# Kernel optimization log

Measured on AMD Instinct MI355X. Metric: run time of the kernel, lower is better.

Reference implementation:

```python
import jax, jax.numpy as jnp
import numpy as np

B, O, L, T = 1024, 50, 20, 10
D, H, V = 64, 128, 49688
DM, FF = 2 * H, 4 * H  # transformer d_model=256, ffn=512


def _ln(x, g, b, eps=1e-5):
    m = x.mean(-1, keepdims=True)
    v = ((x - m) ** 2).mean(-1, keepdims=True)
    return (x - m) / jnp.sqrt(v + eps) * g + b


def _mha(x, in_w, in_b, out_w, out_b, nh):
    # x: [..., S, d]; torch nn.MultiheadAttention with packed qkv in_proj
    lead, S, d = x.shape[:-2], x.shape[-2], x.shape[-1]
    hd = d // nh
    qkv = x @ in_w.T + in_b
    q, k, v = jnp.split(qkv, 3, axis=-1)
    q = q.reshape(*lead, S, nh, hd)
    k = k.reshape(*lead, S, nh, hd)
    v = v.reshape(*lead, S, nh, hd)
    sc = jnp.einsum('...qhd,...khd->...hqk', q, k) / jnp.sqrt(jnp.asarray(hd, x.dtype))
    a = jax.nn.softmax(sc, axis=-1)
    o = jnp.einsum('...hqk,...khd->...qhd', a, v).reshape(*lead, S, d)
    return o @ out_w.T + out_b


def _gru_dir(x_seq, wi, wh, bi, bh):
    # x_seq: [O, B, D] -> outputs [O, B, H]; PyTorch GRU cell equations
    def step(h, x):
        gi = x @ wi.T + bi
        gh = h @ wh.T + bh
        i_r, i_z, i_n = jnp.split(gi, 3, axis=-1)
        h_r, h_z, h_n = jnp.split(gh, 3, axis=-1)
        r = jax.nn.sigmoid(i_r + h_r)
        z = jax.nn.sigmoid(i_z + h_z)
        n = jnp.tanh(i_n + r * h_n)
        h2 = (1.0 - z) * n + z * h
        return h2, h2
    h0 = jnp.zeros((x_seq.shape[1], wh.shape[1]), x_seq.dtype)
    _, ys = jax.lax.scan(step, h0, x_seq)
    return ys


def setup_inputs() -> dict:
    key = jax.random.key(0)
    ks = jax.random.split(key, 20)
    rn = lambda k, shape: jax.random.normal(k, shape, jnp.float32) * 0.05
    return {
        'order_history': jax.random.randint(ks[0], (B, O, L), 0, V, jnp.int32),
        'days_between': jax.random.uniform(ks[1], (B, T), jnp.float32) * 30.0,
        'days_since_last': jax.random.uniform(ks[2], (B,), jnp.float32) * 30.0,
        'item_emb': rn(ks[3], (V + 1, D)).at[0].set(0.0),  # padding_idx=0
        'ia_in_w': rn(ks[4], (3 * D, D)), 'ia_in_b': jnp.zeros(3 * D),
        'ia_out_w': rn(ks[5], (D, D)), 'ia_out_b': jnp.zeros(D),
        'gf_wi': rn(ks[6], (3 * H, D)), 'gf_wh': rn(ks[7], (3 * H, H)),
        'gf_bi': jnp.zeros(3 * H), 'gf_bh': jnp.zeros(3 * H),
        'gb_wi': rn(ks[8], (3 * H, D)), 'gb_wh': rn(ks[9], (3 * H, H)),
        'gb_bi': jnp.zeros(3 * H), 'gb_bh': jnp.zeros(3 * H),
        'ta_in_w': rn(ks[10], (3 * DM, DM)), 'ta_in_b': jnp.zeros(3 * DM),
        'ta_out_w': rn(ks[11], (DM, DM)), 'ta_out_b': jnp.zeros(DM),
        't_ln1_g': jnp.ones(DM), 't_ln1_b': jnp.zeros(DM),
        't_ln2_g': jnp.ones(DM), 't_ln2_b': jnp.zeros(DM),
        't_ff1_w': rn(ks[12], (FF, DM)), 't_ff1_b': jnp.zeros(FF),
        't_ff2_w': rn(ks[13], (DM, FF)), 't_ff2_b': jnp.zeros(DM),
        'te1_w': rn(ks[14], (H // 4, 2)), 'te1_b': jnp.zeros(H // 4),
        'te_ln1_g': jnp.ones(H // 4), 'te_ln1_b': jnp.zeros(H // 4),
        'te2_w': rn(ks[15], (H // 2, H // 4)), 'te2_b': jnp.zeros(H // 2),
        'te_ln2_g': jnp.ones(H // 2), 'te_ln2_b': jnp.zeros(H // 2),
        'c_w': rn(ks[16], (H, DM + H // 2)), 'c_b': jnp.zeros(H),
        'c_ln_g': jnp.ones(H), 'c_ln_b': jnp.zeros(H),
    }


def reference(order_history, days_between, days_since_last, item_emb,
              ia_in_w, ia_in_b, ia_out_w, ia_out_b,
              gf_wi, gf_wh, gf_bi, gf_bh, gb_wi, gb_wh, gb_bi, gb_bh,
              ta_in_w, ta_in_b, ta_out_w, ta_out_b,
              t_ln1_g, t_ln1_b, t_ln2_g, t_ln2_b,
              t_ff1_w, t_ff1_b, t_ff2_w, t_ff2_b,
              te1_w, te1_b, te_ln1_g, te_ln1_b, te2_w, te2_b, te_ln2_g, te_ln2_b,
              c_w, c_b, c_ln_g, c_ln_b):
    # per-order item embedding + self-attention + mean pool (batched over B,O)
    E = item_emb[order_history]                            # [B,O,L,D]
    A = _mha(E, ia_in_w, ia_in_b, ia_out_w, ia_out_b, 4)   # [B,O,L,D]
    order_emb = A.mean(axis=2)                             # [B,O,D]
    # bidirectional GRU over order sequence
    x = jnp.transpose(order_emb, (1, 0, 2))                # [O,B,D]
    yf = _gru_dir(x, gf_wi, gf_wh, gf_bi, gf_bh)
    yb = _gru_dir(x[::-1], gb_wi, gb_wh, gb_bi, gb_bh)[::-1]
    g = jnp.transpose(jnp.concatenate([yf, yb], axis=-1), (1, 0, 2))  # [B,O,2H]
    # post-norm TransformerEncoderLayer (dropout inactive at eval)
    sa = _mha(g, ta_in_w, ta_in_b, ta_out_w, ta_out_b, 4)
    h1 = _ln(g + sa, t_ln1_g, t_ln1_b)
    ff = jax.nn.relu(h1 @ t_ff1_w.T + t_ff1_b) @ t_ff2_w.T + t_ff2_b
    h2 = _ln(h1 + ff, t_ln2_g, t_ln2_b)
    order_enc = h2.mean(axis=1)                            # [B,2H]
    # temporal features: mean(days_between), recency (days_std is unused in original)
    feat = jnp.stack([days_between.mean(axis=1), days_since_last], axis=1)  # [B,2]
    t1 = jax.nn.relu(_ln(feat @ te1_w.T + te1_b, te_ln1_g, te_ln1_b))
    t2 = jax.nn.relu(_ln(t1 @ te2_w.T + te2_b, te_ln2_g, te_ln2_b))        # [B,H//2]
    u = jnp.concatenate([order_enc, t2], axis=1)           # [B,2H+H//2]
    return jax.nn.relu(_ln(u @ c_w.T + c_b, c_ln_g, c_ln_b))  # [B,H]
```

## Files before the change

### kernel.cpp

```cpp
#include <hip/hip_runtime.h>


#define B_ 1024
#define O_ 50
#define VROWS 49689
#define VPAD  49792

typedef __attribute__((ext_vector_type(8))) short  short8v;
typedef __attribute__((ext_vector_type(4))) short  short4v;
typedef __attribute__((ext_vector_type(8))) unsigned short ushort8v;
typedef __attribute__((ext_vector_type(4))) unsigned short ushort4v;
typedef __attribute__((ext_vector_type(4))) float f32x4;

__device__ __forceinline__ float sig_(float x)  { return 1.0f / (1.0f + __expf(-x)); }
__device__ __forceinline__ float tanh_(float x) { return 2.0f / (1.0f + __expf(-2.0f * x)) - 1.0f; }

__device__ __forceinline__ unsigned short f2bf(float f) {
  union { float f; unsigned int u; } v; v.f = f;
  unsigned int r = v.u + 0x7FFFu + ((v.u >> 16) & 1u);
  return (unsigned short)(r >> 16);
}
__device__ __forceinline__ float bf2f(unsigned short u) {
  union { unsigned int u; float f; } v; v.u = ((unsigned int)u) << 16;
  return v.f;
}
__device__ __forceinline__ unsigned int pk2bf(float lo, float hi) {
  return (unsigned int)f2bf(lo) | ((unsigned int)f2bf(hi) << 16);
}

__global__ void k_transpose(const float* __restrict__ src, float* __restrict__ dst, int R, int C) {
  int i = blockIdx.x * 256 + threadIdx.x;
  if (i < R * C) {
    int r = i / C, c = i - r * C;
    dst[c * R + r] = src[i];
  }
}

__global__ void k_f32bf16(const float* __restrict__ src, unsigned short* __restrict__ dst, int n) {
  int i = blockIdx.x * 256 + threadIdx.x;
  if (i < n) dst[i] = f2bf(src[i]);
}

__global__ void k_fill_u16(unsigned short* __restrict__ dst, int n) {
  int i = blockIdx.x * 256 + threadIdx.x;
  if (i < n) dst[i] = 0;
}

__global__ void k_pad_bias(const float* __restrict__ src, float* __restrict__ dst,
                           int ns, int nt) {
  int i = blockIdx.x * 256 + threadIdx.x;
  if (i < nt) dst[i] = (i < ns) ? src[i] : 0.f;
}

__global__ void k_cat_bias(const float* __restrict__ a, const float* __restrict__ b,
                           float* __restrict__ dst) {
  int i = blockIdx.x * 256 + threadIdx.x;
  if (i < 768) dst[i] = (i < 384) ? a[i] : b[i - 384];
}

template<int RELU>
__global__ __launch_bounds__(256) void k_gemm128(
    const unsigned short* __restrict__ A, int lda,
    const unsigned short* __restrict__ W, int K,
    const float* __restrict__ bias,
    unsigned short* __restrict__ C, int ldc, int Mclamp)
{
  __shared__ unsigned short As[128 * 40];
  __shared__ unsigned short Bs[128 * 40];
  int n0 = blockIdx.x * 128, m0 = blockIdx.y * 128;
  int t = threadIdx.x, wv = t >> 6, lane = t & 63;
  int fr = lane & 15, kg = lane >> 4;
  int wr = wv >> 1, wc = wv & 1;
  int sr = t >> 1, sc = (t & 1) * 16;

  f32x4 acc[4][4];
#pragma unroll
  for (int mi = 0; mi < 4; ++mi)
#pragma unroll
    for (int ni = 0; ni < 4; ++ni) acc[mi][ni] = (f32x4){0.f, 0.f, 0.f, 0.f};

  int arow = m0 + sr; if (arow >= Mclamp) arow = Mclamp - 1;
  const unsigned short* ga = &A[(size_t)arow * lda + sc];
  const unsigned short* gw = &W[(size_t)(n0 + sr) * K + sc];

  for (int k0 = 0; k0 < K; k0 += 32) {
    ushort8v a0 = *(const ushort8v*)(ga + k0);
    ushort8v a1 = *(const ushort8v*)(ga + k0 + 8);
    ushort8v b0 = *(const ushort8v*)(gw + k0);
    ushort8v b1 = *(const ushort8v*)(gw + k0 + 8);
    __syncthreads();
    *(ushort8v*)&As[sr * 40 + sc]     = a0;
    *(ushort8v*)&As[sr * 40 + sc + 8] = a1;
    *(ushort8v*)&Bs[sr * 40 + sc]     = b0;
    *(ushort8v*)&Bs[sr * 40 + sc + 8] = b1;
    __syncthreads();
    short8v af[4], bfv[4];
#pragma unroll
    for (int mi = 0; mi < 4; ++mi)
      af[mi] = *(const short8v*)&As[(wr * 64 + mi * 16 + fr) * 40 + kg * 8];
#pragma unroll
    for (int ni = 0; ni < 4; ++ni)
      bfv[ni] = *(const short8v*)&Bs[(wc * 64 + ni * 16 + fr) * 40 + kg * 8];
#pragma unroll
    for (int mi = 0; mi < 4; ++mi)
#pragma unroll
      for (int ni = 0; ni < 4; ++ni)
        acc[mi][ni] = __builtin_amdgcn_mfma_f32_16x16x32_bf16(af[mi], bfv[ni], acc[mi][ni], 0, 0, 0);
  }

#pragma unroll
  for (int ni = 0; ni < 4; ++ni) {
    int col = n0 + wc * 64 + ni * 16 + fr;
    float bb = bias[col];
#pragma unroll
    for (int mi = 0; mi < 4; ++mi) {
#pragma unroll
      for (int r = 0; r < 4; ++r) {
        int row = m0 + wr * 64 + mi * 16 + kg * 4 + r;
        float v = acc[mi][ni][r] + bb;
        if (RELU) v = fmaxf(v, 0.f);
        C[(size_t)row * ldc + col] = f2bf(v);
      }
    }
  }
}

__global__ __launch_bounds__(256) void k_item_fused(
    const int* __restrict__ oh,
    const unsigned short* __restrict__ QKVall ,
    const float* __restrict__ wo , const float* __restrict__ bob,
    unsigned short* __restrict__ X )
{
  __shared__ __align__(16) unsigned short QKs[2][20][144];
  __shared__ __align__(16) unsigned short VTs[2][64][36];
  __shared__ __align__(16) unsigned short Ps[4][24][36];
  __shared__ __align__(16) float mAs[2][68];
  __shared__ int ids[2][20];

  int t = threadIdx.x, wv = t >> 6, lane = t & 63;
  int fr = lane & 15, lg = lane >> 4;
  int pr = wv >> 1, half = wv & 1;

  if (t < 40) ids[t / 20][t % 20] = oh[(size_t)(blockIdx.x * 2 + t / 20) * 20 + (t % 20)];
  {
    unsigned int* vz = (unsigned int*)&VTs[t >> 7][(t >> 1) & 63][20 + (t & 1) * 8];
    vz[0] = 0; vz[1] = 0; vz[2] = 0; vz[3] = 0;
    for (int e = t; e < 288; e += 256) {
      int w2 = e / 72, rem = e - w2 * 72;
      *(unsigned int*)&Ps[w2][20 + rem / 18][(rem - (rem / 18) * 18) * 2] = 0;
    }
  }
  __syncthreads();

  for (int e = t; e < 640; e += 256) {
    int pp = e / 320, rem = e - pp * 320;
    int row = rem >> 4, ch = (rem & 15) * 8;
    const unsigned short* src = QKVall + (size_t)ids[pp][row] * 256 + ch;
    *(ushort8v*)&QKs[pp][row][ch] = *(const ushort8v*)src;
  }
  for (int e = t; e < 1280; e += 256) {
    int pp = e / 640, rem = e - pp * 640;
    int jp = rem >> 6, c = rem & 63;
    unsigned int u0 = QKVall[(size_t)ids[pp][2 * jp] * 256 + 128 + c];
    unsigned int u1 = QKVall[(size_t)ids[pp][2 * jp + 1] * 256 + 128 + c];
    *(unsigned int*)&VTs[pp][c][2 * jp] = u0 | (u1 << 16);
  }
  __syncthreads();

  int rj1 = (fr + 16 < 20) ? fr + 16 : 19;
  bool iv1 = fr < 4;
  int pr1 = iv1 ? 16 + fr : 20;
#pragma unroll
  for (int hi = 0; hi < 2; ++hi) {
    int h = half * 2 + hi;
    short8v aK0, aK1, bQ0, bQ1;
    {
      short8v z = {0,0,0,0,0,0,0,0};
      aK0 = z; aK1 = z; bQ0 = z; bQ1 = z;
    }
    if (lg < 2) {
      aK0 = *(const short8v*)&QKs[pr][fr][64 + h * 16 + lg * 8];
      aK1 = *(const short8v*)&QKs[pr][rj1][64 + h * 16 + lg * 8];
      bQ0 = *(const short8v*)&QKs[pr][fr][h * 16 + lg * 8];
      bQ1 = *(const short8v*)&QKs[pr][rj1][h * 16 + lg * 8];
    }
    f32x4 s00 = {0.f,0.f,0.f,0.f}, s01 = {0.f,0.f,0.f,0.f};
    f32x4 s10 = {0.f,0.f,0.f,0.f}, s11 = {0.f,0.f,0.f,0.f};
    s00 = __builtin_amdgcn_mfma_f32_16x16x32_bf16(aK0, bQ0, s00, 0, 0, 0);
    s01 = __builtin_amdgcn_mfma_f32_16x16x32_bf16(aK0, bQ1, s01, 0, 0, 0);
    s10 = __builtin_amdgcn_mfma_f32_16x16x32_bf16(aK1, bQ0, s10, 0, 0, 0);
    s11 = __builtin_amdgcn_mfma_f32_16x16x32_bf16(aK1, bQ1, s11, 0, 0, 0);

    float e00[4], e01[4], e10[4], e11[4];
    float d0 = 0.f, d1 = 0.f;
#pragma unroll
    for (int r = 0; r < 4; ++r) {
      int j1 = 16 + lg * 4 + r;
      bool jv1 = j1 < 20;
      float v00 = __expf(0.25f * s00[r]);
      float v01 = iv1 ? __expf(0.25f * s01[r]) : 0.f;
      float v10 = jv1 ? __expf(0.25f * s10[r]) : 0.f;
      float v11 = (jv1 && iv1) ? __expf(0.25f * s11[r]) : 0.f;
      e00[r] = v00; e01[r] = v01; e10[r] = v10; e11[r] = v11;
      d0 += v00 + v10; d1 += v01 + v11;
    }
    d0 += __shfl_xor(d0, 16, 64); d0 += __shfl_xor(d0, 32, 64);
    d1 += __shfl_xor(d1, 16, 64); d1 += __shfl_xor(d1, 32, 64);
    float inv0 = __fdividef(1.f, d0);
    float inv1 = iv1 ? __fdividef(1.f, d1) : 0.f;

    *(unsigned int*)&Ps[wv][fr][lg * 4]          = pk2bf(e00[0]*inv0, e00[1]*inv0);
    *(unsigned int*)&Ps[wv][fr][lg * 4 + 2]      = pk2bf(e00[2]*inv0, e00[3]*inv0);
    *(unsigned int*)&Ps[wv][fr][16 + lg * 4]     = pk2bf(e10[0]*inv0, e10[1]*inv0);
    *(unsigned int*)&Ps[wv][fr][16 + lg * 4 + 2] = pk2bf(e10[2]*inv0, e10[3]*inv0);
    if (iv1) {
      *(unsigned int*)&Ps[wv][16 + fr][lg * 4]          = pk2bf(e01[0]*inv1, e01[1]*inv1);
      *(unsigned int*)&Ps[wv][16 + fr][lg * 4 + 2]      = pk2bf(e01[2]*inv1, e01[3]*inv1);
      *(unsigned int*)&Ps[wv][16 + fr][16 + lg * 4]     = pk2bf(e11[0]*inv1, e11[1]*inv1);
      *(unsigned int*)&Ps[wv][16 + fr][16 + lg * 4 + 2] = pk2bf(e11[2]*inv1, e11[3]*inv1);
    }

    short8v pa0, pa1, bV;
    {
      short4v l0 = *(const short4v*)&Ps[wv][fr][lg * 8];
      short4v h0 = *(const short4v*)&Ps[wv][fr][lg * 8 + 4];
      short4v l1 = *(const short4v*)&Ps[wv][pr1][lg * 8];
      short4v h1 = *(const short4v*)&Ps[wv][pr1][lg * 8 + 4];
      short4v lv = *(const short4v*)&VTs[pr][h * 16 + fr][lg * 8];
      short4v hv = *(const short4v*)&VTs[pr][h * 16 + fr][lg * 8 + 4];
      pa0[0]=l0[0]; pa0[1]=l0[1]; pa0[2]=l0[2]; pa0[3]=l0[3];
      pa0[4]=h0[0]; pa0[5]=h0[1]; pa0[6]=h0[2]; pa0[7]=h0[3];
      pa1[0]=l1[0]; pa1[1]=l1[1]; pa1[2]=l1[2]; pa1[3]=l1[3];
      pa1[4]=h1[0]; pa1[5]=h1[1]; pa1[6]=h1[2]; pa1[7]=h1[3];
      bV[0]=lv[0]; bV[1]=lv[1]; bV[2]=lv[2]; bV[3]=lv[3];
      bV[4]=hv[0]; bV[5]=hv[1]; bV[6]=hv[2]; bV[7]=hv[3];
    }
    f32x4 m20 = {0.f,0.f,0.f,0.f}, m21 = {0.f,0.f,0.f,0.f};
    m20 = __builtin_amdgcn_mfma_f32_16x16x32_bf16(pa0, bV, m20, 0, 0, 0);
    m21 = __builtin_amdgcn_mfma_f32_16x16x32_bf16(pa1, bV, m21, 0, 0, 0);

    float sm = m20[0] + m20[1] + m20[2] + m20[3];
    if (lg == 0) sm += m21[0] + m21[1] + m21[2] + m21[3];
    sm += __shfl_xor(sm, 16, 64);
    sm += __shfl_xor(sm, 32, 64);
    if (lg == 0) mAs[pr][h * 16 + fr] = sm * 0.05f;
  }
  __syncthreads();

  if (t < 128) {
    int p2 = t >> 6, col = t & 63;
    float acc = bob[col];
    const float* wrow = &wo[(size_t)col * 64];
    for (int k = 0; k < 64; k += 4) {
      float4 m4 = *(const float4*)&mAs[p2][k];
      float4 w4 = *(const float4*)(wrow + k);
      acc += m4.x * w4.x + m4.y * w4.y + m4.z * w4.z + m4.w * w4.w;
    }
    X[(size_t)(blockIdx.x * 2 + p2) * 64 + col] = f2bf(acc);
  }
}

__global__ __launch_bounds__(512) void k_gru_mfma(
    const unsigned short* __restrict__ GI,
    const unsigned short* __restrict__ whf,
    const unsigned short* __restrict__ whb,
    const float* __restrict__ bh_f, const float* __restrict__ bh_b,
    unsigned short* __restrict__ G )
{
  __shared__ unsigned short hsb[16][136];
  __shared__ float ah[4][392];

  int bid = blockIdx.x;
  int dir = bid >> 8;
  int rg  = bid & 255;
  const unsigned short* wh = dir ? whb : whf;
  const float* bh = dir ? bh_b : bh_f;

  int t = threadIdx.x;
  int w = t >> 6, lane = t & 63;
  int fr = lane & 15, kg = lane >> 4;

  short8v bfr[3][4];
#pragma unroll
  for (int n = 0; n < 3; ++n)
#pragma unroll
    for (int kf = 0; kf < 4; ++kf)
      bfr[n][kf] = *(const short8v*)&wh[(size_t)(w * 48 + n * 16 + fr) * 128 + kf * 32 + kg * 8];

  for (int e = t; e < 16 * 136; e += 512) ((unsigned short*)hsb)[e] = 0;

  int grow = t >> 7, gc = t & 127;
  float bh0 = bh[gc], bh1 = bh[128 + gc], bh2 = bh[256 + gc];
  float hold = 0.f;
  const unsigned short* gip = &GI[(size_t)(rg * 4 + grow) * 50 * 768 + dir * 384];
  unsigned short* gout = &G[((size_t)(rg * 4 + grow) * 50) * 256 + dir * 128 + gc];

  __syncthreads();

  int o0 = dir ? 49 : 0;
  unsigned short c0v = gip[(size_t)o0 * 768 + gc];
  unsigned short c1v = gip[(size_t)o0 * 768 + 128 + gc];
  unsigned short c2v = gip[(size_t)o0 * 768 + 256 + gc];

  for (int s = 0; s < 50; ++s) {
    int o  = dir ? 49 - s : s;
    unsigned short n0v = 0, n1v = 0, n2v = 0;
    if (s < 49) {
      int on = dir ? 48 - s : s + 1;
      n0v = gip[(size_t)on * 768 + gc];
      n1v = gip[(size_t)on * 768 + 128 + gc];
      n2v = gip[(size_t)on * 768 + 256 + gc];
    }

    short8v a0 = *(const short8v*)&hsb[fr][0 * 32 + kg * 8];
    short8v a1 = *(const short8v*)&hsb[fr][1 * 32 + kg * 8];
    short8v a2 = *(const short8v*)&hsb[fr][2 * 32 + kg * 8];
    short8v a3 = *(const short8v*)&hsb[fr][3 * 32 + kg * 8];

    f32x4 acc0 = {0.f,0.f,0.f,0.f}, acc1 = {0.f,0.f,0.f,0.f}, acc2 = {0.f,0.f,0.f,0.f};
    acc0 = __builtin_amdgcn_mfma_f32_16x16x32_bf16(a0, bfr[0][0], acc0, 0, 0, 0);
    acc1 = __builtin_amdgcn_mfma_f32_16x16x32_bf16(a0, bfr[1][0], acc1, 0, 0, 0);
    acc2 = __builtin_amdgcn_mfma_f32_16x16x32_bf16(a0, bfr[2][0], acc2, 0, 0, 0);
    acc0 = __builtin_amdgcn_mfma_f32_16x16x32_bf16(a1, bfr[0][1], acc0, 0, 0, 0);
    acc1 = __builtin_amdgcn_mfma_f32_16x16x32_bf16(a1, bfr[1][1], acc1, 0, 0, 0);
    acc2 = __builtin_amdgcn_mfma_f32_16x16x32_bf16(a1, bfr[2][1], acc2, 0, 0, 0);
    acc0 = __builtin_amdgcn_mfma_f32_16x16x32_bf16(a2, bfr[0][2], acc0, 0, 0, 0);
    acc1 = __builtin_amdgcn_mfma_f32_16x16x32_bf16(a2, bfr[1][2], acc1, 0, 0, 0);
    acc2 = __builtin_amdgcn_mfma_f32_16x16x32_bf16(a2, bfr[2][2], acc2, 0, 0, 0);
    acc0 = __builtin_amdgcn_mfma_f32_16x16x32_bf16(a3, bfr[0][3], acc0, 0, 0, 0);
    acc1 = __builtin_amdgcn_mfma_f32_16x16x32_bf16(a3, bfr[1][3], acc1, 0, 0, 0);
    acc2 = __builtin_amdgcn_mfma_f32_16x16x32_bf16(a3, bfr[2][3], acc2, 0, 0, 0);

    if (kg == 0) {
#pragma unroll
      for (int r = 0; r < 4; ++r) {
        ah[r][w * 48 + 0 * 16 + fr] = acc0[r];
        ah[r][w * 48 + 1 * 16 + fr] = acc1[r];
        ah[r][w * 48 + 2 * 16 + fr] = acc2[r];
      }
    }
    __syncthreads();

    float ai0 = bf2f(c0v), ai1 = bf2f(c1v), ai2 = bf2f(c2v);
    float ah0 = ah[grow][gc] + bh0;
    float ah1 = ah[grow][128 + gc] + bh1;
    float ah2 = ah[grow][256 + gc] + bh2;
    float rr = sig_(ai0 + ah0);
    float zz = sig_(ai1 + ah1);
    float nn = tanh_(ai2 + rr * ah2);
    float h2 = (1.f - zz) * nn + zz * hold;
    hold = h2;
    unsigned short hb = f2bf(h2);
    hsb[grow][gc] = hb;
    gout[(size_t)o * 256] = hb;
    c0v = n0v; c1v = n1v; c2v = n2v;
    __syncthreads();
  }
}

__global__ __launch_bounds__(256) void k_attn_core(unsigned short* __restrict__ BIG)
{
  __shared__ __align__(16) float qs[50][68], ks[50][68], vs[50][68];
  __shared__ float P[50][52];
  int bl = blockIdx.x >> 2, h = blockIdx.x & 3;
  int t = threadIdx.x;
  size_t base = (size_t)bl * 50 * 768;
  int hc = h * 64;

  for (int e = t; e < 800; e += 256) {
    int row = e >> 4, c4 = (e & 15) * 4;
    ushort4v q4 = *(const ushort4v*)&BIG[base + (size_t)row * 768 + hc + c4];
    ushort4v k4 = *(const ushort4v*)&BIG[base + (size_t)row * 768 + 256 + hc + c4];
    ushort4v v4 = *(const ushort4v*)&BIG[base + (size_t)row * 768 + 512 + hc + c4];
#pragma unroll
    for (int j = 0; j < 4; ++j) {
      qs[row][c4 + j] = bf2f(q4[j]);
      ks[row][c4 + j] = bf2f(k4[j]);
      vs[row][c4 + j] = bf2f(v4[j]);
    }
  }
  __syncthreads();

  for (int e = t; e < 2500; e += 256) {
    int i = e / 50, j = e - (e / 50) * 50;
    float d = 0.f;
#pragma unroll
    for (int k = 0; k < 64; k += 4) {
      float4 q = *(const float4*)&qs[i][k];
      float4 kk = *(const float4*)&ks[j][k];
      d += q.x * kk.x + q.y * kk.y + q.z * kk.z + q.w * kk.w;
    }
    P[i][j] = d * 0.125f;
  }
  __syncthreads();

  {
    int l = t & 31, rslot = t >> 5;
    for (int i0 = 0; i0 < 50; i0 += 8) {
      int i = i0 + rslot;
      if (i < 50) {
        float p1 = P[i][l];
        float p2 = (l < 18) ? P[i][l + 32] : -1e30f;
        float m = fmaxf(p1, p2);
#pragma unroll
        for (int d2 = 1; d2 < 32; d2 <<= 1) m = fmaxf(m, __shfl_xor(m, d2, 32));
        float e1 = __expf(p1 - m);
        float e2 = (l < 18) ? __expf(p2 - m) : 0.f;
        float s = e1 + e2;
#pragma unroll
        for (int d2 = 1; d2 < 32; d2 <<= 1) s += __shfl_xor(s, d2, 32);
        float inv = __fdividef(1.f, s);
        P[i][l] = e1 * inv;
        if (l < 18) P[i][l + 32] = e2 * inv;
      }
    }
  }
  __syncthreads();
  for (int e = t; e < 1600; e += 256) {
    int i = e >> 5, c2 = (e & 31) * 2;
    float a0 = 0.f, a1 = 0.f;
    for (int j = 0; j < 50; ++j) {
      float pv = P[i][j];
      a0 += pv * vs[j][c2];
      a1 += pv * vs[j][c2 + 1];
    }
    *(unsigned int*)&BIG[base + (size_t)i * 768 + hc + c2] = pk2bf(a0, a1);
  }
}

__global__ __launch_bounds__(256) void k_ln_res(
    const unsigned short* __restrict__ res, const unsigned short* __restrict__ add,
    int addld, unsigned short* __restrict__ dst,
    const float* __restrict__ g, const float* __restrict__ bt)
{
  int row = blockIdx.x * 4 + (threadIdx.x >> 6);
  int lane = threadIdx.x & 63;
  int c = lane * 4;
  ushort4v rv = *(const ushort4v*)&res[(size_t)row * 256 + c];
  ushort4v av = *(const ushort4v*)&add[(size_t)row * addld + c];
  float x0 = bf2f(rv[0]) + bf2f(av[0]);
  float x1 = bf2f(rv[1]) + bf2f(av[1]);
  float x2 = bf2f(rv[2]) + bf2f(av[2]);
  float x3 = bf2f(rv[3]) + bf2f(av[3]);
  float s = x0 + x1 + x2 + x3;
  float sq = x0 * x0 + x1 * x1 + x2 * x2 + x3 * x3;
#pragma unroll
  for (int d = 1; d < 64; d <<= 1) { s += __shfl_xor(s, d, 64); sq += __shfl_xor(sq, d, 64); }
  float m = s * (1.f / 256.f);
  float var = sq * (1.f / 256.f) - m * m;
  float rs = rsqrtf(var + 1e-5f);
  float4 gv = *(const float4*)&g[c];
  float4 bv = *(const float4*)&bt[c];
  ushort4v ov;
  ov[0] = f2bf((x0 - m) * rs * gv.x + bv.x);
  ov[1] = f2bf((x1 - m) * rs * gv.y + bv.y);
  ov[2] = f2bf((x2 - m) * rs * gv.z + bv.z);
  ov[3] = f2bf((x3 - m) * rs * gv.w + bv.w);
  *(ushort4v*)&dst[(size_t)row * 256 + c] = ov;
}

__global__ __launch_bounds__(256) void k_heads(
    const unsigned short* __restrict__ H2 ,
    const float* __restrict__ daysb, const float* __restrict__ dayss,
    const float* __restrict__ te1_w, const float* __restrict__ te1_b,
    const float* __restrict__ ln1g, const float* __restrict__ ln1b,
    const float* __restrict__ te2_w, const float* __restrict__ te2_b,
    const float* __restrict__ ln2g, const float* __restrict__ ln2b,
    const float* __restrict__ cWT ,
    const float* __restrict__ c_b, const float* __restrict__ clng,
    const float* __restrict__ clnb, float* __restrict__ out)
{
  __shared__ float oe[256];
  __shared__ float feat[2];
  __shared__ float s1[32], s2[64], pre[128], stat[2];
  int b = blockIdx.x, t = threadIdx.x;
  {
    float s = 0.f;
    for (int o = 0; o < 50; ++o) s += bf2f(H2[((size_t)b * 50 + o) * 256 + t]);
    oe[t] = s * 0.02f;
  }
  if (t == 0) {
    float f0 = 0.f;
    for (int i = 0; i < 10; ++i) f0 += daysb[b * 10 + i];
    feat[0] = f0 * 0.1f;
    feat[1] = dayss[b];
  }
  __syncthreads();
  if (t < 32) s1[t] = te1_b[t] + feat[0] * te1_w[2 * t] + feat[1] * te1_w[2 * t + 1];
  __syncthreads();
  if (t == 0) {
    float s = 0.f; for (int j = 0; j < 32; ++j) s += s1[j];
    float m = s * (1.f / 32.f);
    float v = 0.f; for (int j = 0; j < 32; ++j) { float d = s1[j] - m; v += d * d; }
    stat[0] = m; stat[1] = rsqrtf(v * (1.f / 32.f) + 1e-5f);
  }
  __syncthreads();
  if (t < 32) s1[t] = fmaxf((s1[t] - stat[0]) * stat[1] * ln1g[t] + ln1b[t], 0.f);
  __syncthreads();
  if (t < 64) {
    float a = te2_b[t];
    for (int k = 0; k < 32; ++k) a += s1[k] * te2_w[t * 32 + k];
    s2[t] = a;
  }
  __syncthreads();
  if (t == 0) {
    float s = 0.f; for (int j = 0; j < 64; ++j) s += s2[j];
    float m = s * (1.f / 64.f);
    float v = 0.f; for (int j = 0; j < 64; ++j) { float d = s2[j] - m; v += d * d; }
    stat[0] = m; stat[1] = rsqrtf(v * (1.f / 64.f) + 1e-5f);
  }
  __syncthreads();
  if (t < 64) s2[t] = fmaxf((s2[t] - stat[0]) * stat[1] * ln2g[t] + ln2b[t], 0.f);
  __syncthreads();
  if (t < 128) {
    float p = c_b[t];
    for (int k = 0; k < 256; ++k) p += oe[k] * cWT[k * 128 + t];
    for (int k = 0; k < 64; ++k)  p += s2[k] * cWT[(256 + k) * 128 + t];
    pre[t] = p;
  }
  __syncthreads();
  if (t == 0) {
    float s = 0.f; for (int j = 0; j < 128; ++j) s += pre[j];
    float m = s * (1.f / 128.f);
    float v = 0.f; for (int j = 0; j < 128; ++j) { float d = pre[j] - m; v += d * d; }
    stat[0] = m; stat[1] = rsqrtf(v * (1.f / 128.f) + 1e-5f);
  }
  __syncthreads();
  if (t < 128)
    out[(size_t)b * 128 + t] = fmaxf((pre[t] - stat[0]) * stat[1] * clng[t] + clnb[t], 0.f);
}

extern "C" void kernel_launch(void* const* d_in, const int* in_sizes, int n_in,
                              void* d_out, int out_size, void* d_ws, size_t ws_size,
                              hipStream_t stream)
{
  const int*   oh       = (const int*)d_in[0];
  const float* daysb    = (const float*)d_in[1];
  const float* dayss    = (const float*)d_in[2];
  const float* emb      = (const float*)d_in[3];
  const float* ia_in_w  = (const float*)d_in[4];
  const float* ia_in_b  = (const float*)d_in[5];
  const float* ia_out_w = (const float*)d_in[6];
  const float* ia_out_b = (const float*)d_in[7];
  const float* gf_wi = (const float*)d_in[8];
  const float* gf_wh = (const float*)d_in[9];
  const float* gf_bi = (const float*)d_in[10];
  const float* gf_bh = (const float*)d_in[11];
  const float* gb_wi = (const float*)d_in[12];
  const float* gb_wh = (const float*)d_in[13];
  const float* gb_bi = (const float*)d_in[14];
  const float* gb_bh = (const float*)d_in[15];
  const float* ta_in_w  = (const float*)d_in[16];
  const float* ta_in_b  = (const float*)d_in[17];
  const float* ta_out_w = (const float*)d_in[18];
  const float* ta_out_b = (const float*)d_in[19];
  const float* t_ln1_g = (const float*)d_in[20];
  const float* t_ln1_b = (const float*)d_in[21];
  const float* t_ln2_g = (const float*)d_in[22];
  const float* t_ln2_b = (const float*)d_in[23];
  const float* t_ff1_w = (const float*)d_in[24];
  const float* t_ff1_b = (const float*)d_in[25];
  const float* t_ff2_w = (const float*)d_in[26];
  const float* t_ff2_b = (const float*)d_in[27];
  const float* te1_w = (const float*)d_in[28];
  const float* te1_b = (const float*)d_in[29];
  const float* te_ln1_g = (const float*)d_in[30];
  const float* te_ln1_b = (const float*)d_in[31];
  const float* te2_w = (const float*)d_in[32];
  const float* te2_b = (const float*)d_in[33];
  const float* te_ln2_g = (const float*)d_in[34];
  const float* te_ln2_b = (const float*)d_in[35];
  const float* c_w   = (const float*)d_in[36];
  const float* c_b   = (const float*)d_in[37];
  const float* c_ln_g = (const float*)d_in[38];
  const float* c_ln_b = (const float*)d_in[39];

  float* ws = (float*)d_ws;
  const size_t OFF_GB   = 0;
  const size_t OFF_X    = 6553600;
  const size_t OFF_S    = OFF_X + 1638400;
  const size_t OW_C     = OFF_S + 19660800;
  const size_t OW_BC    = OW_C + 40960;
  const size_t OW_BQ    = OW_BC + 768;
  const size_t OW_BF    = OW_BQ + 256;
  const size_t OW_EMB   = OW_BF + 344064;
  const size_t TOTAL    = OW_EMB + 1590048;
  if (ws_size < TOTAL * sizeof(float)) return;

  unsigned short* Gb = (unsigned short*)(ws + OFF_GB);
  unsigned short* Xb = (unsigned short*)(ws + OFF_X);
  float* w_c  = ws + OW_C;
  float* biascat = ws + OW_BC;
  float* biasq   = ws + OW_BQ;
  unsigned short* bfp = (unsigned short*)(ws + OW_BF);
  unsigned short* b_ta_in  = bfp;
  unsigned short* b_ta_out = b_ta_in + 196608;
  unsigned short* b_ff1    = b_ta_out + 65536;
  unsigned short* b_ff2    = b_ff1 + 131072;
  unsigned short* b_qkvw   = b_ff2 + 131072;
  unsigned short* b_wi_f   = b_qkvw + 16384;
  unsigned short* b_wi_b   = b_wi_f + 24576;
  unsigned short* b_wh_f   = b_wi_b + 24576;
  unsigned short* b_wh_b   = b_wh_f + 49152;
  unsigned short* embb = (unsigned short*)(ws + OW_EMB);

  unsigned short* QKVall = (unsigned short*)(ws + OFF_S);
  unsigned short* GI     = (unsigned short*)(ws + OFF_S);
  unsigned short* BIGb   = (unsigned short*)(ws + OFF_S);

  k_transpose<<<(320 * 128 + 255) / 256, 256, 0, stream>>>(c_w, w_c, 128, 320);
  k_cat_bias<<<3, 256, 0, stream>>>(gf_bi, gb_bi, biascat);
  k_pad_bias<<<1, 256, 0, stream>>>(ia_in_b, biasq, 192, 256);
  #define CV(SRC, DST, N) k_f32bf16<<<((N)+255)/256, 256, 0, stream>>>(SRC, DST, N)
  CV(ta_in_w,  b_ta_in,  196608);
  CV(ta_out_w, b_ta_out, 65536);
  CV(t_ff1_w,  b_ff1,    131072);
  CV(t_ff2_w,  b_ff2,    131072);
  CV(ia_in_w,  b_qkvw,   12288);
  CV(gf_wi,    b_wi_f,   24576);
  CV(gb_wi,    b_wi_b,   24576);
  CV(gf_wh,    b_wh_f,   49152);
  CV(gb_wh,    b_wh_b,   49152);
  CV(emb,      embb,     3180096);
  #undef CV
  k_fill_u16<<<(4096 + 255) / 256, 256, 0, stream>>>(b_qkvw + 12288, 4096);

  k_gemm128<0><<<dim3(256 / 128, VPAD / 128), 256, 0, stream>>>(
      embb, 64, b_qkvw, 64, biasq, QKVall, 256, VROWS);

  k_item_fused<<<B_ * O_ / 2, 256, 0, stream>>>(oh, QKVall, ia_out_w, ia_out_b, Xb);

  k_gemm128<0><<<dim3(768 / 128, 51200 / 128), 256, 0, stream>>>(
      Xb, 64, b_wi_f , 64, biascat, GI, 768, 51200);
  k_gru_mfma<<<512, 512, 0, stream>>>(GI, b_wh_f, b_wh_b, gf_bh, gb_bh, Gb);

  k_gemm128<0><<<dim3(768 / 128, 51200 / 128), 256, 0, stream>>>(
      Gb, 256, b_ta_in, 256, ta_in_b, BIGb, 768, 51200);
  k_attn_core<<<B_ * 4, 256, 0, stream>>>(BIGb);
  k_gemm128<0><<<dim3(256 / 128, 51200 / 128), 256, 0, stream>>>(
      BIGb, 768, b_ta_out, 256, ta_out_b, BIGb + 256, 768, 51200);
  k_ln_res<<<51200 / 4, 256, 0, stream>>>(Gb, BIGb + 256, 768, Gb, t_ln1_g, t_ln1_b);
  k_gemm128<1><<<dim3(512 / 128, 51200 / 128), 256, 0, stream>>>(
      Gb, 256, b_ff1, 256, t_ff1_b, BIGb, 768, 51200);
  k_gemm128<0><<<dim3(256 / 128, 51200 / 128), 256, 0, stream>>>(
      BIGb, 768, b_ff2, 512, t_ff2_b, BIGb + 512, 768, 51200);
  k_ln_res<<<51200 / 4, 256, 0, stream>>>(Gb, BIGb + 512, 768, Gb, t_ln2_g, t_ln2_b);

  k_heads<<<B_, 256, 0, stream>>>(Gb, daysb, dayss, te1_w, te1_b, te_ln1_g, te_ln1_b,
                                  te2_w, te2_b, te_ln2_g, te_ln2_b,
                                  w_c, c_b, c_ln_g, c_ln_b, (float*)d_out);
}
```

Measured before the change: 622.6 us.

## Batch prep kernels into two launches and stage V rows via LDS

The five small setup kernels and ten fp32-to-bf16 conversion launches are merged into two kernels: one combined prep kernel and one multi-segment conversion kernel driven by a struct of pointers. This is meant to cut launch overhead and the small-kernel tail gaps. Separately, the item-attention kernel now loads V rows with 16-byte vector loads into LDS aliased over the P buffer, then transposes them in LDS into VTs. This replaces scattered 2-byte global gathers, at the cost of an extra barrier and zeroing the P padding after the transpose.

```diff
diff --git a/kernel.cpp b/kernel.cpp
--- a/kernel.cpp
+++ b/kernel.cpp
@@ -28,34 +28,37 @@
   return (unsigned int)f2bf(lo) | ((unsigned int)f2bf(hi) << 16);
 }
 
-__global__ void k_transpose(const float* __restrict__ src, float* __restrict__ dst, int R, int C) {
+struct CvArgs {
+  const float* src[10];
+  unsigned short* dst[10];
+  int n[10];
+};
+__global__ void k_cv_multi(CvArgs a) {
   int i = blockIdx.x * 256 + threadIdx.x;
-  if (i < R * C) {
-    int r = i / C, c = i - r * C;
-    dst[c * R + r] = src[i];
-  }
-}
-
-__global__ void k_f32bf16(const float* __restrict__ src, unsigned short* __restrict__ dst, int n) {
+#pragma unroll
+  for (int s = 0; s < 10; ++s) {
+    if (i < a.n[s]) { a.dst[s][i] = f2bf(a.src[s][i]); return; }
+    i -= a.n[s];
+  }
+}
+
+__global__ void k_prep_small(const float* __restrict__ c_w, float* __restrict__ w_c,
+                             const float* __restrict__ bia, const float* __restrict__ bib,
+                             float* __restrict__ biascat,
+                             const float* __restrict__ qb, float* __restrict__ biasq,
+                             unsigned short* __restrict__ wpad) {
   int i = blockIdx.x * 256 + threadIdx.x;
-  if (i < n) dst[i] = f2bf(src[i]);
-}
-
-__global__ void k_fill_u16(unsigned short* __restrict__ dst, int n) {
-  int i = blockIdx.x * 256 + threadIdx.x;
-  if (i < n) dst[i] = 0;
-}
-
-__global__ void k_pad_bias(const float* __restrict__ src, float* __restrict__ dst,
-                           int ns, int nt) {
-  int i = blockIdx.x * 256 + threadIdx.x;
-  if (i < nt) dst[i] = (i < ns) ? src[i] : 0.f;
-}
-
-__global__ void k_cat_bias(const float* __restrict__ a, const float* __restrict__ b,
-                           float* __restrict__ dst) {
-  int i = blockIdx.x * 256 + threadIdx.x;
-  if (i < 768) dst[i] = (i < 384) ? a[i] : b[i - 384];
+  if (i < 40960) {
+    int r = i / 320, c = i - r * 320;
+    w_c[c * 128 + r] = c_w[i];
+    return;
+  }
+  i -= 40960;
+  if (i < 768) { biascat[i] = (i < 384) ? bia[i] : bib[i - 384]; return; }
+  i -= 768;
+  if (i < 256) { biasq[i] = (i < 192) ? qb[i] : 0.f; return; }
+  i -= 256;
+  if (i < 4096) wpad[i] = 0;
 }
 
 template<int RELU>
@@ -140,15 +143,12 @@
   int t = threadIdx.x, wv = t >> 6, lane = t & 63;
   int fr = lane & 15, lg = lane >> 4;
   int pr = wv >> 1, half = wv & 1;
+  unsigned short (*Vs)[20][72] = (unsigned short (*)[20][72])&Ps[0][0][0];
 
   if (t < 40) ids[t / 20][t % 20] = oh[(size_t)(blockIdx.x * 2 + t / 20) * 20 + (t % 20)];
   {
     unsigned int* vz = (unsigned int*)&VTs[t >> 7][(t >> 1) & 63][20 + (t & 1) * 8];
     vz[0] = 0; vz[1] = 0; vz[2] = 0; vz[3] = 0;
-    for (int e = t; e < 288; e += 256) {
-      int w2 = e / 72, rem = e - w2 * 72;
-      *(unsigned int*)&Ps[w2][20 + rem / 18][(rem - (rem / 18) * 18) * 2] = 0;
-    }
   }
   __syncthreads();
 
@@ -158,14 +158,28 @@
     const unsigned short* src = QKVall + (size_t)ids[pp][row] * 256 + ch;
     *(ushort8v*)&QKs[pp][row][ch] = *(const ushort8v*)src;
   }
-  for (int e = t; e < 1280; e += 256) {
-    int pp = e / 640, rem = e - pp * 640;
-    int jp = rem >> 6, c = rem & 63;
-    unsigned int u0 = QKVall[(size_t)ids[pp][2 * jp] * 256 + 128 + c];
-    unsigned int u1 = QKVall[(size_t)ids[pp][2 * jp + 1] * 256 + 128 + c];
-    *(unsigned int*)&VTs[pp][c][2 * jp] = u0 | (u1 << 16);
-  }
-  __syncthreads();
+  for (int e = t; e < 320; e += 256) {
+    int pp = e / 160, rem = e - pp * 160;
+    int row = rem >> 3, ch = (rem & 7) * 8;
+    const unsigned short* src = QKVall + (size_t)ids[pp][row] * 256 + 128 + ch;
+    *(ushort8v*)&Vs[pp][row][ch] = *(const ushort8v*)src;
+  }
+  __syncthreads();
+
+  for (int e = t; e < 640; e += 256) {
+    int pp = e / 320, rem = e - pp * 320;
+    int jp = rem >> 5, c0 = (rem & 31) * 2;
+    unsigned int a = *(const unsigned int*)&Vs[pp][2 * jp][c0];
+    unsigned int b = *(const unsigned int*)&Vs[pp][2 * jp + 1][c0];
+    *(unsigned int*)&VTs[pp][c0][2 * jp]     = (a & 0xFFFFu) | (b << 16);
+    *(unsigned int*)&VTs[pp][c0 + 1][2 * jp] = (a >> 16) | (b & 0xFFFF0000u);
+  }
+  __syncthreads();
+
+  for (int e = lane; e < 72; e += 64) {
+    int row = 20 + e / 18, col = (e - (e / 18) * 18) * 2;
+    *(unsigned int*)&Ps[wv][row][col] = 0;
+  }
 
   int rj1 = (fr + 16 < 20) ? fr + 16 : 19;
   bool iv1 = fr < 4;
@@ -608,22 +622,23 @@
   unsigned short* GI     = (unsigned short*)(ws + OFF_S);
   unsigned short* BIGb   = (unsigned short*)(ws + OFF_S);
 
-  k_transpose<<<(320 * 128 + 255) / 256, 256, 0, stream>>>(c_w, w_c, 128, 320);
-  k_cat_bias<<<3, 256, 0, stream>>>(gf_bi, gb_bi, biascat);
-  k_pad_bias<<<1, 256, 0, stream>>>(ia_in_b, biasq, 192, 256);
-  #define CV(SRC, DST, N) k_f32bf16<<<((N)+255)/256, 256, 0, stream>>>(SRC, DST, N)
-  CV(ta_in_w,  b_ta_in,  196608);
-  CV(ta_out_w, b_ta_out, 65536);
-  CV(t_ff1_w,  b_ff1,    131072);
-  CV(t_ff2_w,  b_ff2,    131072);
-  CV(ia_in_w,  b_qkvw,   12288);
-  CV(gf_wi,    b_wi_f,   24576);
-  CV(gb_wi,    b_wi_b,   24576);
-  CV(gf_wh,    b_wh_f,   49152);
-  CV(gb_wh,    b_wh_b,   49152);
-  CV(emb,      embb,     3180096);
-  #undef CV
-  k_fill_u16<<<(4096 + 255) / 256, 256, 0, stream>>>(b_qkvw + 12288, 4096);
+  k_prep_small<<<(40960 + 768 + 256 + 4096 + 255) / 256, 256, 0, stream>>>(
+      c_w, w_c, gf_bi, gb_bi, biascat, ia_in_b, biasq, b_qkvw + 12288);
+  {
+    CvArgs a;
+    a.src[0] = ta_in_w;  a.dst[0] = b_ta_in;  a.n[0] = 196608;
+    a.src[1] = ta_out_w; a.dst[1] = b_ta_out; a.n[1] = 65536;
+    a.src[2] = t_ff1_w;  a.dst[2] = b_ff1;    a.n[2] = 131072;
+    a.src[3] = t_ff2_w;  a.dst[3] = b_ff2;    a.n[3] = 131072;
+    a.src[4] = ia_in_w;  a.dst[4] = b_qkvw;   a.n[4] = 12288;
+    a.src[5] = gf_wi;    a.dst[5] = b_wi_f;   a.n[5] = 24576;
+    a.src[6] = gb_wi;    a.dst[6] = b_wi_b;   a.n[6] = 24576;
+    a.src[7] = gf_wh;    a.dst[7] = b_wh_f;   a.n[7] = 49152;
+    a.src[8] = gb_wh;    a.dst[8] = b_wh_b;   a.n[8] = 49152;
+    a.src[9] = emb;      a.dst[9] = embb;     a.n[9] = 3180096;
+    int total = 196608 + 65536 + 131072 + 131072 + 12288 + 24576 + 24576 + 49152 + 49152 + 3180096;
+    k_cv_multi<<<(total + 255) / 256, 256, 0, stream>>>(a);
+  }
 
   k_gemm128<0><<<dim3(256 / 128, VPAD / 128), 256, 0, stream>>>(
       embb, 64, b_qkvw, 64, biasq, QKVall, 256, VROWS);
```

Result: faster. 576.9 us (-7.3%).
